# Kernel optimization log

Hardware: AMD Instinct MI355X
Metric: run time of the kernel (lower is better)

Reference implementation:

```python
import jax, jax.numpy as jnp
import numpy as np

B, N, D, H, K = 1, 8192, 1024, 512, 100
R = 0.3
EPS = 1e-12  # torch F.normalize eps


def setup_inputs() -> dict:
    key = jax.random.key(0)
    ks = jax.random.split(key, 10)
    s_in = 1.0 / np.sqrt(D)
    s_wa = 1.0 / np.sqrt(2 * K)
    s_h = 1.0 / np.sqrt(H)
    return {
        "x_q": jax.random.normal(ks[0], (B, N, D), jnp.float32),
        "x_k": jax.random.normal(ks[1], (B, N, D), jnp.float32),
        "WQ_w": jax.random.uniform(ks[2], (D, H), jnp.float32, -s_in, s_in),
        "WQ_b": jax.random.uniform(ks[3], (H,), jnp.float32, -s_in, s_in),
        "WK_w": jax.random.uniform(ks[4], (D, H), jnp.float32, -s_in, s_in),
        "WK_b": jax.random.uniform(ks[5], (H,), jnp.float32, -s_in, s_in),
        "WA_w": jax.random.uniform(ks[6], (2 * K, 1), jnp.float32, -s_wa, s_wa),
        "WA_b": jax.random.uniform(ks[7], (1,), jnp.float32, -s_wa, s_wa),
        "cls_w": jax.random.uniform(ks[8], (H, 1), jnp.float32, -s_h, s_h),
        "cls_b": jax.random.uniform(ks[9], (1,), jnp.float32, -s_h, s_h),
    }


def reference(x_q, x_k, WQ_w, WQ_b, WK_w, WK_b, WA_w, WA_b, cls_w, cls_b):
    query = jnp.tanh(x_q @ WQ_w + WQ_b)          # [B,N,H]
    keyt = jnp.tanh(x_k @ WK_w + WK_b)           # [B,N,H]
    qn = query / jnp.maximum(jnp.linalg.norm(query, axis=2, keepdims=True), EPS)
    kn = keyt / jnp.maximum(jnp.linalg.norm(keyt, axis=2, keepdims=True), EPS)
    A = jnp.einsum('bnh,bmh->bnm', qn, kn)       # [B,N,N] cosine sims
    # sorted(A)[..., -100:] == top-100 in ascending order
    top, _ = jax.lax.top_k(A, K)                 # descending
    A1 = top[..., ::-1]                          # ascending, matches torch slice
    Acmb = -(jnp.concatenate([A1, A1 * A1], axis=-1) @ WA_w + WA_b)  # [B,N,1]
    # rank-based threshold from batch 0 (thre = sorted scores at index N-int(r*N))
    thre = jnp.sort(Acmb[0, :, 0])[N - int(R * N)]
    Acmb = jnp.where(Acmb > thre, Acmb, 0.0)     # F.threshold (strict >)
    Acmb = jax.nn.softmax(Acmb, axis=1)          # softmax over instances
    Aw = jnp.transpose(Acmb, (0, 2, 1))          # [B,1,N]
    z = (Aw @ query).reshape(-1, H)              # [B,H]
    Y_prob = z @ cls_w + cls_b                   # [B,1]
    return (Y_prob, Aw)
```

## Files before the change

### kernel.cpp

```cpp
#include <hip/hip_runtime.h>
#include <hip/hip_bf16.h>
#include <math.h>

#define NTOK 8192
#define DIM  1024
#define HDIM 512
#define KTOP 100
#define CHUNK 4096
#define KTH_RANK 2457
#define EQCAP 2048
#define PADK 0x3FFFFFFFu

typedef float f32x4 __attribute__((ext_vector_type(4)));
typedef short bf16x8 __attribute__((ext_vector_type(8)));
typedef unsigned int u32;
typedef unsigned short u16;

__device__ __forceinline__ unsigned key_of(float f) {
  unsigned u = __float_as_uint(f);
  return (u & 0x80000000u) ? ~u : (u | 0x80000000u);
}
__device__ __forceinline__ float float_of_key(unsigned key) {
  unsigned u = (key & 0x80000000u) ? (key ^ 0x80000000u) : ~key;
  return __uint_as_float(u);
}
__device__ __forceinline__ u16 bf16_rn(float x) {
  unsigned u = __float_as_uint(x);
  return (u16)((u + 0x7FFFu + ((u >> 16) & 1u)) >> 16);
}
__device__ __forceinline__ float bf16f(u16 h) {
  return __uint_as_float(((unsigned)h) << 16);
}
__device__ __forceinline__ void gload16(const void* gptr, void* lptr) {
  __builtin_amdgcn_global_load_lds(
      (const __attribute__((address_space(1))) u32*)gptr,
      (__attribute__((address_space(3))) u32*)lptr, 16, 0, 0);
}

template<int MODE, int FM>
__global__ __launch_bounds__(512, 4) void gemm_hl(
    const u16* __restrict__ Ahi, const u16* __restrict__ Alo,
    const u16* __restrict__ Bhi, const u16* __restrict__ Blo,
    float* __restrict__ Cf, u16* __restrict__ Chi, u16* __restrict__ Clo,
    const float* __restrict__ bias,
    const float* __restrict__ rq, const float* __restrict__ rk,
    int K, int ldc)
{
  constexpr int BM = FM * 32;
  constexpr int RT = 2 * BM + 256;
  constexpr int RPW = RT / 8;
  constexpr int NI = RPW / 16;
  __shared__ __align__(16) short lds[2][RT * 32];

  const int tid = threadIdx.x, lane = tid & 63, wave = tid >> 6;
  const int wm = wave >> 2, wn = wave & 3;

  const int nwg = gridDim.x * gridDim.y;
  const int lin = blockIdx.y * gridDim.x + blockIdx.x;
  const int cpx = nwg >> 3;
  const int swz = (lin & 7) * cpx + (lin >> 3);
  const int bx = swz % gridDim.x, by = swz / gridDim.x;
  const int bm = by * BM, bn = bx * 128;

  f32x4 acc[FM][2] = {};

  auto STAGE = [&](int buf, int k0) {
#pragma unroll
    for (int j = 0; j < NI; ++j) {
      int rg = wave * RPW + j * 16;
      int r  = rg + (lane >> 2);
      const u16* gp; size_t grow;
      if (rg < BM)                { gp = Ahi; grow = (size_t)(bm + r); }
      else if (rg < 2 * BM)       { gp = Alo; grow = (size_t)(bm + r - BM); }
      else if (rg < 2 * BM + 128) { gp = Bhi; grow = (size_t)(bn + r - 2 * BM); }
      else                        { gp = Blo; grow = (size_t)(bn + r - 2 * BM - 128); }
      int ks = k0 + (((lane & 3) ^ ((r >> 1) & 3)) << 3);
      gload16(gp + grow * (size_t)K + ks, &lds[buf][rg * 32]);
    }
  };

  STAGE(0, 0);
  __syncthreads();
  const int NT = K / 32;
  int cur = 0;
  for (int t = 0; t < NT; ++t) {
    if (t + 1 < NT) STAGE(cur ^ 1, (t + 1) * 32);
    const short* L = lds[cur];
    const int qb = lane >> 4;
    bf16x8 ah[FM], al[FM], bh[2], bl[2];
#pragma unroll
    for (int m = 0; m < FM; ++m) {
      int r = wm * (FM * 16) + m * 16 + (lane & 15);
      int off = r * 32 + ((qb ^ ((r >> 1) & 3)) << 3);
      ah[m] = *(const bf16x8*)&L[off];
      al[m] = *(const bf16x8*)&L[BM * 32 + off];
    }
#pragma unroll
    for (int n = 0; n < 2; ++n) {
      int r = wn * 32 + n * 16 + (lane & 15);
      int off = r * 32 + ((qb ^ ((r >> 1) & 3)) << 3);
      bh[n] = *(const bf16x8*)&L[2 * BM * 32 + off];
      bl[n] = *(const bf16x8*)&L[(2 * BM + 128) * 32 + off];
    }
#pragma unroll
    for (int n = 0; n < 2; ++n)
#pragma unroll
      for (int m = 0; m < FM; ++m) {
        acc[m][n] = __builtin_amdgcn_mfma_f32_16x16x32_bf16(ah[m], bh[n], acc[m][n], 0, 0, 0);
        acc[m][n] = __builtin_amdgcn_mfma_f32_16x16x32_bf16(ah[m], bl[n], acc[m][n], 0, 0, 0);
        acc[m][n] = __builtin_amdgcn_mfma_f32_16x16x32_bf16(al[m], bh[n], acc[m][n], 0, 0, 0);
      }
    __syncthreads();
    cur ^= 1;
  }

#pragma unroll
  for (int m = 0; m < FM; ++m) {
    int rbase = bm + wm * (FM * 16) + m * 16 + (lane >> 4) * 4;
#pragma unroll
    for (int n = 0; n < 2; ++n) {
      int col = bn + wn * 32 + n * 16 + (lane & 15);
      if (MODE == 0) {
        float cs = rk[col];
#pragma unroll
        for (int r = 0; r < 4; ++r)
          Cf[(size_t)(rbase + r) * ldc + col] = acc[m][n][r] * rq[rbase + r] * cs;
      } else {
        float b = bias[col];
#pragma unroll
        for (int r = 0; r < 4; ++r) {
          size_t idx = (size_t)(rbase + r) * ldc + col;
          float t = tanhf(acc[m][n][r] + b);
          if (MODE == 1) Cf[idx] = t;
          u16 h = bf16_rn(t);
          Chi[idx] = h;
          Clo[idx] = bf16_rn(t - bf16f(h));
        }
      }
    }
  }
}

__global__ __launch_bounds__(256) void xsplit(
    const float* __restrict__ x, u16* __restrict__ hi, u16* __restrict__ lo)
{
  for (int i = blockIdx.x * 256 + threadIdx.x; i < NTOK * DIM / 4; i += gridDim.x * 256) {
    float4 v = ((const float4*)x)[i];
    ushort4 h, l;
    h.x = bf16_rn(v.x); l.x = bf16_rn(v.x - bf16f(h.x));
    h.y = bf16_rn(v.y); l.y = bf16_rn(v.y - bf16f(h.y));
    h.z = bf16_rn(v.z); l.z = bf16_rn(v.z - bf16f(h.z));
    h.w = bf16_rn(v.w); l.w = bf16_rn(v.w - bf16f(h.w));
    ((ushort4*)hi)[i] = h;
    ((ushort4*)lo)[i] = l;
  }
}

__global__ __launch_bounds__(256) void wt_cast(
    const float* __restrict__ W, u16* __restrict__ Thi, u16* __restrict__ Tlo)
{
  __shared__ float t[32][33];
  const int bx = blockIdx.x, by = blockIdx.y;
  const int r = threadIdx.x >> 5, c = threadIdx.x & 31;
#pragma unroll
  for (int i = 0; i < 4; ++i)
    t[r + i * 8][c] = W[(size_t)(by * 32 + r + i * 8) * HDIM + bx * 32 + c];
  __syncthreads();
#pragma unroll
  for (int i = 0; i < 4; ++i) {
    int n = bx * 32 + r + i * 8, k = by * 32 + c;
    float v = t[c][r + i * 8];
    u16 h = bf16_rn(v);
    Thi[(size_t)n * DIM + k] = h;
    Tlo[(size_t)n * DIM + k] = bf16_rn(v - bf16f(h));
  }
}

__global__ __launch_bounds__(256) void rownorm_inv(
    const u16* __restrict__ qh, const u16* __restrict__ ql,
    const u16* __restrict__ kh, const u16* __restrict__ kl,
    float* __restrict__ rq, float* __restrict__ rk)
{
  const int half = blockIdx.x >> 11;
  const int row = (blockIdx.x & 2047) * 4 + (threadIdx.x >> 6);
  const int lane = threadIdx.x & 63;
  const u16* hi = half ? kh : qh;
  const u16* lo = half ? kl : ql;
  size_t base = (size_t)row * HDIM + lane * 8;
  ushort4 h0 = *(const ushort4*)&hi[base], h1 = *(const ushort4*)&hi[base + 4];
  ushort4 l0 = *(const ushort4*)&lo[base], l1 = *(const ushort4*)&lo[base + 4];
  float f[8] = {bf16f(h0.x)+bf16f(l0.x), bf16f(h0.y)+bf16f(l0.y),
                bf16f(h0.z)+bf16f(l0.z), bf16f(h0.w)+bf16f(l0.w),
                bf16f(h1.x)+bf16f(l1.x), bf16f(h1.y)+bf16f(l1.y),
                bf16f(h1.z)+bf16f(l1.z), bf16f(h1.w)+bf16f(l1.w)};
  float ss = 0.f;
#pragma unroll
  for (int j = 0; j < 8; ++j) ss += f[j] * f[j];
#pragma unroll
  for (int off = 32; off > 0; off >>= 1) ss += __shfl_xor(ss, off);
  if (lane == 0) {
    float r = 1.0f / fmaxf(sqrtf(ss), 1e-12f);
    (half ? rk : rq)[row] = r;
  }
}

__global__ __launch_bounds__(256) void topk_acmb(
    const float* __restrict__ Arows, const float* __restrict__ WA_w,
    const float* __restrict__ WA_b, float* __restrict__ Acmb, int row_base)
{
  __shared__ u32 hist[2048];
  __shared__ u32 eqbuf[EQCAP];
  __shared__ u32 grbuf[128];
  __shared__ u32 tsum[256], tabove[256];
  __shared__ u32 s_b, s_need, s_cb, s_b2, s_need2, s_cb2, s_cg, s_ce;

  const int tid = threadIdx.x;
  const float4* src = (const float4*)(Arows + (size_t)blockIdx.x * NTOK);

  for (int i = tid; i < 2048; i += 256) hist[i] = 0u;
  if (tid == 0) { s_cg = 0u; s_ce = 0u; }

  u32 keys[32];
#pragma unroll
  for (int i = 0; i < 8; ++i) {
    float4 v = src[i * 256 + tid];
    keys[i * 4 + 0] = key_of(v.x);
    keys[i * 4 + 1] = key_of(v.y);
    keys[i * 4 + 2] = key_of(v.z);
    keys[i * 4 + 3] = key_of(v.w);
  }
  __syncthreads();

#pragma unroll
  for (int j = 0; j < 32; ++j) {
    u32 bin = keys[j] >> 20;
    atomicAdd(&hist[bin >> 1], (bin & 1) ? 0x10000u : 1u);
  }
  __syncthreads();

  auto scan12 = [&](u32 needK, u32* ob, u32* oneed, u32* ocb) {
    u32 cnt[16]; u32 mysum = 0;
#pragma unroll
    for (int i = 0; i < 8; ++i) {
      u32 pk = hist[tid * 8 + i];
      u32 c0 = pk & 0xFFFFu, c1 = pk >> 16;
      cnt[2 * i] = c0; cnt[2 * i + 1] = c1; mysum += c0 + c1;
    }
    tsum[tid] = mysum;
    __syncthreads();
    if (tid < 64) {
      u32 s0 = tsum[tid * 4], s1 = tsum[tid * 4 + 1];
      u32 s2 = tsum[tid * 4 + 2], s3 = tsum[tid * 4 + 3];
      u32 lsum = s0 + s1 + s2 + s3;
      u32 suf = lsum;
#pragma unroll
      for (int d = 1; d < 64; d <<= 1) {
        u32 v = (u32)__shfl_down((int)suf, d);
        if (tid + d < 64) suf += v;
      }
      u32 above = suf - lsum;
      tabove[tid * 4 + 3] = above;
      tabove[tid * 4 + 2] = above + s3;
      tabove[tid * 4 + 1] = above + s3 + s2;
      tabove[tid * 4 + 0] = above + s3 + s2 + s1;
    }
    __syncthreads();
    u32 above = tabove[tid];
#pragma unroll
    for (int b = 15; b >= 0; --b) {
      u32 c = cnt[b];
      if (above < needK && above + c >= needK) {
        *ob = (u32)(tid * 16 + b); *oneed = needK - above; *ocb = c;
      }
      above += c;
    }
    __syncthreads();
  };
  scan12(KTOP, &s_b, &s_need, &s_cb);

  const u32 b1 = s_b;
  const u32 need1 = s_need, cb1 = s_cb;
  const bool two = (cb1 > EQCAP);
  u32 b2v = 0, needF = need1;
  if (two) {
    for (int i = tid; i < 2048; i += 256) hist[i] = 0u;
    __syncthreads();
#pragma unroll
    for (int j = 0; j < 32; ++j) {
      u32 k = keys[j];
      if ((k >> 20) == b1) {
        u32 bin = (k >> 8) & 0xFFFu;
        atomicAdd(&hist[bin >> 1], (bin & 1) ? 0x10000u : 1u);
      }
    }
    __syncthreads();
    scan12(need1, &s_b2, &s_need2, &s_cb2);
    b2v = s_b2; needF = s_need2;
  }

#pragma unroll
  for (int j = 0; j < 32; ++j) {
    u32 k = keys[j];
    u32 hi12 = k >> 20;
    bool g = hi12 > b1, e = (hi12 == b1);
    if (two) {
      u32 mid = (k >> 8) & 0xFFFu;
      g = g || (e && mid > b2v);
      e = e && (mid == b2v);
    }
    if (g) { u32 p = atomicAdd(&s_cg, 1u); if (p < 128u) grbuf[p] = k; }
    else if (e) { u32 p = atomicAdd(&s_ce, 1u); if (p < EQCAP) eqbuf[p] = k; }
  }
  __syncthreads();

  const u32 cg = s_cg;
  const u32 ce = min(s_ce, (u32)EQCAP);
  const bool small = (ce <= 128u);

  auto sortnet = [&](u32& a, u32& b, bool asc) {
    const int lane = tid;
    for (int k = 2; k <= 128; k <<= 1) {
      for (int j = k >> 1; j > 0; j >>= 1) {
        if (j == 64) {
          bool up = ((lane & k) == 0) == asc;
          u32 lo = min(a, b), hi = max(a, b);
          a = up ? lo : hi;  b = up ? hi : lo;
        } else {
          bool upa = ((lane & k) == 0) == asc;
          bool upb = (((lane + 64) & k) == 0) == asc;
          bool lowa = (lane & j) == 0;
          u32 oa = (u32)__shfl_xor((int)a, j);
          u32 ob = (u32)__shfl_xor((int)b, j);
          a = (lowa == upa) ? min(a, oa) : max(a, oa);
          b = (lowa == upb) ? min(b, ob) : max(b, ob);
        }
      }
    }
  };

  if (tid < 64 && small) {
    u32 e0 = (tid < (int)ce) ? eqbuf[tid] : PADK;
    u32 e1 = (tid + 64 < (int)ce) ? eqbuf[tid + 64] : PADK;
    sortnet(e0, e1, false);
    eqbuf[tid] = e0; eqbuf[tid + 64] = e1;
  }
  __syncthreads();

  if (tid < 64) {
    if (!small) {
      for (u32 itn = 0; itn < needF; ++itn) {
        u32 mx = 0u;
        for (u32 i = tid; i < ce; i += 64) mx = max(mx, eqbuf[i]);
#pragma unroll
        for (int d = 32; d > 0; d >>= 1) mx = max(mx, (u32)__shfl_xor((int)mx, d));
        u32 fidx = 0xFFFFFFFFu;
        for (u32 i = tid; i < ce; i += 64) if (eqbuf[i] == mx) fidx = min(fidx, i);
#pragma unroll
        for (int d = 32; d > 0; d >>= 1) fidx = min(fidx, (u32)__shfl_xor((int)fidx, d));
        if (tid == (int)(fidx & 63u)) eqbuf[fidx] = 0u;
        if (tid == 0) grbuf[cg + itn] = mx;
      }
    }
    int i0 = tid, i1 = tid + 64;
    u32 m0, m1;
    if (small) {
      m0 = (i0 < (int)cg) ? grbuf[i0] : ((i0 < KTOP) ? eqbuf[i0 - cg] : PADK);
      m1 = (i1 < (int)cg) ? grbuf[i1] : ((i1 < KTOP) ? eqbuf[i1 - cg] : PADK);
    } else {
      m0 = (i0 < KTOP) ? grbuf[i0] : PADK;
      m1 = (i1 < KTOP) ? grbuf[i1] : PADK;
    }
    sortnet(m0, m1, true);
    float s = 0.f;
    if (i0 >= 28) {
      float a1 = float_of_key(m0);
      int t = i0 - 28;
      s += a1 * WA_w[t] + a1 * a1 * WA_w[KTOP + t];
    }
    {
      float a1 = float_of_key(m1);
      int t = i1 - 28;
      s += a1 * WA_w[t] + a1 * a1 * WA_w[KTOP + t];
    }
#pragma unroll
    for (int d = 32; d > 0; d >>= 1) s += __shfl_xor(s, d);
    if (tid == 0) Acmb[row_base + (int)blockIdx.x] = -(s + WA_b[0]);
  }
}

__global__ __launch_bounds__(1024) void thr_softmax(
    const float* __restrict__ Acmb, float* __restrict__ out)
{
  __shared__ float vals[NTOK];
  __shared__ unsigned hist[256];
  __shared__ unsigned sufs[256];
  __shared__ float red[1024];
  __shared__ unsigned s_prefix, s_need;
  const int tid = threadIdx.x;
#pragma unroll
  for (int s = 0; s < 8; ++s) vals[tid + s * 1024] = Acmb[tid + s * 1024];
  if (tid == 0) { s_prefix = 0u; s_need = KTH_RANK; }
  __syncthreads();

  for (int pass = 3; pass >= 0; --pass) {
    if (tid < 256) hist[tid] = 0u;
    __syncthreads();
    unsigned pref  = s_prefix;
    unsigned pmask = (pass == 3) ? 0u : (0xFFFFFFFFu << ((pass + 1) * 8));
#pragma unroll
    for (int s = 0; s < 8; ++s) {
      unsigned key = key_of(vals[tid + s * 1024]);
      if ((key & pmask) == pref)
        atomicAdd(&hist[(key >> (pass * 8)) & 255u], 1u);
    }
    __syncthreads();
    if (tid < 256) sufs[tid] = hist[tid];
    __syncthreads();
    for (int off = 1; off < 256; off <<= 1) {
      unsigned add = 0u;
      if (tid < 256 && tid + off < 256) add = sufs[tid + off];
      __syncthreads();
      if (tid < 256) sufs[tid] += add;
      __syncthreads();
    }
    unsigned need = s_need;
    __syncthreads();
    if (tid < 256) {
      unsigned above = (tid == 255) ? 0u : sufs[tid + 1];
      if (sufs[tid] >= need && above < need) {
        s_prefix = pref | ((unsigned)tid << (pass * 8));
        s_need   = need - above;
      }
    }
    __syncthreads();
  }
  const float thre = float_of_key(s_prefix);

  float loc[8]; float mx = -1e30f;
#pragma unroll
  for (int s = 0; s < 8; ++s) {
    float v = vals[tid + s * 1024];
    v = (v > thre) ? v : 0.0f;
    loc[s] = v; mx = fmaxf(mx, v);
  }
  red[tid] = mx; __syncthreads();
  for (int off = 512; off > 0; off >>= 1) {
    if (tid < off) red[tid] = fmaxf(red[tid], red[tid + off]);
    __syncthreads();
  }
  float m = red[0]; __syncthreads();
  float sm = 0.0f;
#pragma unroll
  for (int s = 0; s < 8; ++s) sm += expf(loc[s] - m);
  red[tid] = sm; __syncthreads();
  for (int off = 512; off > 0; off >>= 1) {
    if (tid < off) red[tid] += red[tid + off];
    __syncthreads();
  }
  float Z = red[0];
#pragma unroll
  for (int s = 0; s < 8; ++s)
    out[1 + tid + s * 1024] = expf(loc[s] - m) / Z;
}

__global__ __launch_bounds__(256) void z_partial(
    const float* __restrict__ aw, const float* __restrict__ query,
    float* __restrict__ zpart)
{
  const int g = blockIdx.x, t = threadIdx.x;
  float a0 = 0.f, a1 = 0.f;
  for (int r = 0; r < 64; ++r) {
    int n = g * 64 + r;
    float w = aw[n];
    const float* q = query + (size_t)n * HDIM;
    a0 = fmaf(w, q[t],       a0);
    a1 = fmaf(w, q[t + 256], a1);
  }
  zpart[(size_t)g * HDIM + t]       = a0;
  zpart[(size_t)g * HDIM + t + 256] = a1;
}

__global__ __launch_bounds__(512) void finalize(
    const float* __restrict__ zpart, const float* __restrict__ cls_w,
    const float* __restrict__ cls_b, float* __restrict__ out)
{
  __shared__ float red[512];
  const int t = threadIdx.x;
  float s = 0.f;
  for (int g = 0; g < 128; ++g) s += zpart[(size_t)g * HDIM + t];
  red[t] = s * cls_w[t];
  __syncthreads();
  for (int off = 256; off > 0; off >>= 1) {
    if (t < off) red[t] += red[t + off];
    __syncthreads();
  }
  if (t == 0) out[0] = red[0] + cls_b[0];
}

extern "C" void kernel_launch(void* const* d_in, const int* in_sizes, int n_in,
                              void* d_out, int out_size, void* d_ws, size_t ws_size,
                              hipStream_t stream) {
  (void)in_sizes; (void)n_in; (void)out_size; (void)ws_size;
  const float* x_q   = (const float*)d_in[0];
  const float* x_k   = (const float*)d_in[1];
  const float* WQ_w  = (const float*)d_in[2];
  const float* WQ_b  = (const float*)d_in[3];
  const float* WK_w  = (const float*)d_in[4];
  const float* WK_b  = (const float*)d_in[5];
  const float* WA_w  = (const float*)d_in[6];
  const float* WA_b  = (const float*)d_in[7];
  const float* cls_w = (const float*)d_in[8];
  const float* cls_b = (const float*)d_in[9];
  float* out = (float*)d_out;
  char* base = (char*)d_ws;
  const size_t MB = 1u << 20;

  float* query = (float*)(base);
  u16* qh      = (u16*)(base + 16 * MB);
  u16* ql      = (u16*)(base + 24 * MB);
  u16* kh      = (u16*)(base + 32 * MB);
  u16* kl      = (u16*)(base + 40 * MB);
  u16* xs_hi   = (u16*)(base + 48 * MB);
  u16* xs_lo   = (u16*)(base + 64 * MB);
  float* Ach   = (float*)(base + 80 * MB);
  u16* wt_hi   = (u16*)(base + 208 * MB);
  u16* wt_lo   = (u16*)(base + 209 * MB);
  float* rq    = (float*)(base + 210 * MB);
  float* rk    = (float*)(base + 210 * MB + 65536);
  float* Acmb  = (float*)(base + 211 * MB);
  float* zpart = (float*)(base + 211 * MB + 65536);

  dim3 b256(256), b512(512);
  dim3 gproj(HDIM / 128, NTOK / 64);
  dim3 gchunk(NTOK / 128, CHUNK / 128);

  wt_cast<<<dim3(16, 32), b256, 0, stream>>>(WQ_w, wt_hi, wt_lo);
  xsplit<<<2048, b256, 0, stream>>>(x_q, xs_hi, xs_lo);
  gemm_hl<1, 2><<<gproj, b512, 0, stream>>>(xs_hi, xs_lo, wt_hi, wt_lo,
      query, qh, ql, WQ_b, nullptr, nullptr, DIM, HDIM);
  wt_cast<<<dim3(16, 32), b256, 0, stream>>>(WK_w, wt_hi, wt_lo);
  xsplit<<<2048, b256, 0, stream>>>(x_k, xs_hi, xs_lo);
  gemm_hl<2, 2><<<gproj, b512, 0, stream>>>(xs_hi, xs_lo, wt_hi, wt_lo,
      nullptr, kh, kl, WK_b, nullptr, nullptr, DIM, HDIM);
  rownorm_inv<<<4096, b256, 0, stream>>>(qh, ql, kh, kl, rq, rk);
  for (int c = 0; c < NTOK / CHUNK; ++c) {
    gemm_hl<0, 4><<<gchunk, b512, 0, stream>>>(
        qh + (size_t)c * CHUNK * HDIM, ql + (size_t)c * CHUNK * HDIM,
        kh, kl, Ach, nullptr, nullptr, nullptr, rq + c * CHUNK, rk, HDIM, NTOK);
    topk_acmb<<<CHUNK, b256, 0, stream>>>(Ach, WA_w, WA_b, Acmb, c * CHUNK);
  }
  thr_softmax<<<1, dim3(1024), 0, stream>>>(Acmb, out);
  z_partial<<<128, b256, 0, stream>>>(out + 1, query, zpart);
  finalize<<<1, dim3(512), 0, stream>>>(zpart, cls_w, cls_b, out);
}
```

Before: 563.9 us.

## Fuse fp32-to-bf16 hi/lo split into projection GEMM staging and shrink chunk size

The projection GEMMs now read fp32 inputs directly and split them into bf16 hi/lo parts while staging into LDS. This removes the separate xsplit kernels and their round trip of the split arrays through global memory. CHUNK also drops from 4096 to 1024, so the similarity buffer is smaller and more likely to stay in cache, but there are more GEMM and top-k launches with smaller grids. The A-operand staging now uses synchronous loads and ALU conversion in the loop instead of async global-to-LDS loads, which may reduce overlap with compute.

New measurement: 621.1 us. 10.1% more time.

```diff
diff --git a/kernel.cpp b/kernel.cpp
--- a/kernel.cpp
+++ b/kernel.cpp
@@ -6,7 +6,7 @@
 #define DIM  1024
 #define HDIM 512
 #define KTOP 100
-#define CHUNK 4096
+#define CHUNK 1024
 #define KTH_RANK 2457
 #define EQCAP 2048
 #define PADK 0x3FFFFFFFu
@@ -39,6 +39,7 @@
 
 template<int MODE, int FM>
 __global__ __launch_bounds__(512, 4) void gemm_hl(
+    const float* __restrict__ Xf,
     const u16* __restrict__ Ahi, const u16* __restrict__ Alo,
     const u16* __restrict__ Bhi, const u16* __restrict__ Blo,
     float* __restrict__ Cf, u16* __restrict__ Chi, u16* __restrict__ Clo,
@@ -48,8 +49,6 @@
 {
   constexpr int BM = FM * 32;
   constexpr int RT = 2 * BM + 256;
-  constexpr int RPW = RT / 8;
-  constexpr int NI = RPW / 16;
   __shared__ __align__(16) short lds[2][RT * 32];
 
   const int tid = threadIdx.x, lane = tid & 63, wave = tid >> 6;
@@ -65,17 +64,41 @@
   f32x4 acc[FM][2] = {};
 
   auto STAGE = [&](int buf, int k0) {
-#pragma unroll
-    for (int j = 0; j < NI; ++j) {
-      int rg = wave * RPW + j * 16;
-      int r  = rg + (lane >> 2);
-      const u16* gp; size_t grow;
-      if (rg < BM)                { gp = Ahi; grow = (size_t)(bm + r); }
-      else if (rg < 2 * BM)       { gp = Alo; grow = (size_t)(bm + r - BM); }
-      else if (rg < 2 * BM + 128) { gp = Bhi; grow = (size_t)(bn + r - 2 * BM); }
-      else                        { gp = Blo; grow = (size_t)(bn + r - 2 * BM - 128); }
-      int ks = k0 + (((lane & 3) ^ ((r >> 1) & 3)) << 3);
-      gload16(gp + grow * (size_t)K + ks, &lds[buf][rg * 32]);
+    if constexpr (MODE == 0) {
+      constexpr int RPW = RT / 8;
+      constexpr int NI = RPW / 16;
+#pragma unroll
+      for (int j = 0; j < NI; ++j) {
+        int rg = wave * RPW + j * 16;
+        int r  = rg + (lane >> 2);
+        const u16* gp; size_t grow;
+        if (rg < BM)                { gp = Ahi; grow = (size_t)(bm + r); }
+        else if (rg < 2 * BM)       { gp = Alo; grow = (size_t)(bm + r - BM); }
+        else if (rg < 2 * BM + 128) { gp = Bhi; grow = (size_t)(bn + r - 2 * BM); }
+        else                        { gp = Blo; grow = (size_t)(bn + r - 2 * BM - 128); }
+        int ks = k0 + (((lane & 3) ^ ((r >> 1) & 3)) << 3);
+        gload16(gp + grow * (size_t)K + ks, &lds[buf][rg * 32]);
+      }
+    } else {
+#pragma unroll
+      for (int j = 0; j < 2; ++j) {
+        int rg = 2 * BM + wave * 32 + j * 16;
+        int r  = rg + (lane >> 2);
+        const u16* gp; size_t grow;
+        if (rg < 2 * BM + 128) { gp = Bhi; grow = (size_t)(bn + r - 2 * BM); }
+        else                   { gp = Blo; grow = (size_t)(bn + r - 2 * BM - 128); }
+        int ks = k0 + (((lane & 3) ^ ((r >> 1) & 3)) << 3);
+        gload16(gp + grow * (size_t)K + ks, &lds[buf][rg * 32]);
+      }
+      int row = tid >> 3, k4 = (tid & 7) * 4;
+      float4 v = *(const float4*)&Xf[(size_t)(bm + row) * K + k0 + k4];
+      u16 h0 = bf16_rn(v.x), h1 = bf16_rn(v.y), h2 = bf16_rn(v.z), h3 = bf16_rn(v.w);
+      u16 l0 = bf16_rn(v.x - bf16f(h0)), l1 = bf16_rn(v.y - bf16f(h1));
+      u16 l2 = bf16_rn(v.z - bf16f(h2)), l3 = bf16_rn(v.w - bf16f(h3));
+      int q = ((k4 >> 3) ^ ((row >> 1) & 3));
+      int eoff = row * 32 + q * 8 + (k4 & 7);
+      *(ushort4*)&lds[buf][eoff]           = make_ushort4(h0, h1, h2, h3);
+      *(ushort4*)&lds[buf][BM * 32 + eoff] = make_ushort4(l0, l1, l2, l3);
     }
   };
 
@@ -138,21 +161,6 @@
         }
       }
     }
-  }
-}
-
-__global__ __launch_bounds__(256) void xsplit(
-    const float* __restrict__ x, u16* __restrict__ hi, u16* __restrict__ lo)
-{
-  for (int i = blockIdx.x * 256 + threadIdx.x; i < NTOK * DIM / 4; i += gridDim.x * 256) {
-    float4 v = ((const float4*)x)[i];
-    ushort4 h, l;
-    h.x = bf16_rn(v.x); l.x = bf16_rn(v.x - bf16f(h.x));
-    h.y = bf16_rn(v.y); l.y = bf16_rn(v.y - bf16f(h.y));
-    h.z = bf16_rn(v.z); l.z = bf16_rn(v.z - bf16f(h.z));
-    h.w = bf16_rn(v.w); l.w = bf16_rn(v.w - bf16f(h.w));
-    ((ushort4*)hi)[i] = h;
-    ((ushort4*)lo)[i] = l;
   }
 }
 
@@ -520,31 +528,27 @@
   u16* ql      = (u16*)(base + 24 * MB);
   u16* kh      = (u16*)(base + 32 * MB);
   u16* kl      = (u16*)(base + 40 * MB);
-  u16* xs_hi   = (u16*)(base + 48 * MB);
-  u16* xs_lo   = (u16*)(base + 64 * MB);
-  float* Ach   = (float*)(base + 80 * MB);
-  u16* wt_hi   = (u16*)(base + 208 * MB);
-  u16* wt_lo   = (u16*)(base + 209 * MB);
-  float* rq    = (float*)(base + 210 * MB);
-  float* rk    = (float*)(base + 210 * MB + 65536);
-  float* Acmb  = (float*)(base + 211 * MB);
-  float* zpart = (float*)(base + 211 * MB + 65536);
+  float* Ach   = (float*)(base + 48 * MB);
+  u16* wt_hi   = (u16*)(base + 80 * MB);
+  u16* wt_lo   = (u16*)(base + 81 * MB);
+  float* rq    = (float*)(base + 82 * MB);
+  float* rk    = (float*)(base + 82 * MB + 65536);
+  float* Acmb  = (float*)(base + 83 * MB);
+  float* zpart = (float*)(base + 83 * MB + 65536);
 
   dim3 b256(256), b512(512);
   dim3 gproj(HDIM / 128, NTOK / 64);
   dim3 gchunk(NTOK / 128, CHUNK / 128);
 
   wt_cast<<<dim3(16, 32), b256, 0, stream>>>(WQ_w, wt_hi, wt_lo);
-  xsplit<<<2048, b256, 0, stream>>>(x_q, xs_hi, xs_lo);
-  gemm_hl<1, 2><<<gproj, b512, 0, stream>>>(xs_hi, xs_lo, wt_hi, wt_lo,
+  gemm_hl<1, 2><<<gproj, b512, 0, stream>>>(x_q, nullptr, nullptr, wt_hi, wt_lo,
       query, qh, ql, WQ_b, nullptr, nullptr, DIM, HDIM);
   wt_cast<<<dim3(16, 32), b256, 0, stream>>>(WK_w, wt_hi, wt_lo);
-  xsplit<<<2048, b256, 0, stream>>>(x_k, xs_hi, xs_lo);
-  gemm_hl<2, 2><<<gproj, b512, 0, stream>>>(xs_hi, xs_lo, wt_hi, wt_lo,
+  gemm_hl<2, 2><<<gproj, b512, 0, stream>>>(x_k, nullptr, nullptr, wt_hi, wt_lo,
       nullptr, kh, kl, WK_b, nullptr, nullptr, DIM, HDIM);
   rownorm_inv<<<4096, b256, 0, stream>>>(qh, ql, kh, kl, rq, rk);
   for (int c = 0; c < NTOK / CHUNK; ++c) {
-    gemm_hl<0, 4><<<gchunk, b512, 0, stream>>>(
+    gemm_hl<0, 4><<<gchunk, b512, 0, stream>>>(nullptr,
         qh + (size_t)c * CHUNK * HDIM, ql + (size_t)c * CHUNK * HDIM,
         kh, kl, Ach, nullptr, nullptr, nullptr, rq + c * CHUNK, rk, HDIM, NTOK);
     topk_acmb<<<CHUNK, b256, 0, stream>>>(Ach, WA_w, WA_b, Acmb, c * CHUNK);
```
